# Kernel tuning notes

Hardware: AMD Instinct MI355X
Metric: run time of the kernel (lower is better)

The kernel has to match this reference:

```python
import math
import jax, jax.numpy as jnp
import numpy as np

EPS = 1e-5
DIM_E = 448
DIM_H = 64
TOTAL = DIM_E + DIM_H  # 512
C = 1.0


def _project(x, c, margin=1e-3):
    sqrt_c = jnp.sqrt(c)
    norm = jnp.maximum(jnp.linalg.norm(x, axis=-1, keepdims=True), EPS)
    scale = jnp.minimum(((1.0 - margin) / sqrt_c) / norm, 1.0)
    return x * scale


def _mobius_add(x, y, c):
    x2 = jnp.sum(x * x, axis=-1, keepdims=True)
    y2 = jnp.sum(y * y, axis=-1, keepdims=True)
    xy = jnp.sum(x * y, axis=-1, keepdims=True)
    num = (1.0 + 2.0 * c * xy + c * y2) * x + (1.0 - c * x2) * y
    den = jnp.maximum(1.0 + 2.0 * c * xy + c * c * x2 * y2, EPS)
    return _project(num / den, c)


def _exp0(v, c):
    sqrt_c = jnp.sqrt(c)
    norm = jnp.maximum(jnp.linalg.norm(v, axis=-1, keepdims=True), EPS)
    return _project(jnp.tanh(sqrt_c * norm) * v / (sqrt_c * norm), c)


def _dist(x, y, c):
    # x, y broadcast to [B,S,S,dim_h]; returns [B,S,S]
    sqrt_c = jnp.sqrt(c)
    diff = _mobius_add(-x, y, c)
    norm = jnp.minimum(jnp.linalg.norm(diff, axis=-1), (1.0 - 1e-5) / sqrt_c)
    return (2.0 / sqrt_c) * jnp.arctanh(jnp.minimum(sqrt_c * norm, 1.0 - 1e-5))


def setup_inputs() -> dict:
    key = jax.random.key(0)
    ks = jax.random.split(key, 10)
    B, S = 1, 1024
    s = 1.0 / math.sqrt(TOTAL)
    inp = {
        "x": jax.random.normal(ks[0], (B, S, TOTAL), jnp.float32),
        "wq": jax.random.uniform(ks[1], (TOTAL, TOTAL), jnp.float32, -s, s),
        "bq": jax.random.uniform(ks[2], (TOTAL,), jnp.float32, -s, s),
        "wk": jax.random.uniform(ks[3], (TOTAL, TOTAL), jnp.float32, -s, s),
        "bk": jax.random.uniform(ks[4], (TOTAL,), jnp.float32, -s, s),
        "wv": jax.random.uniform(ks[5], (TOTAL, TOTAL), jnp.float32, -s, s),
        "bv": jax.random.uniform(ks[6], (TOTAL,), jnp.float32, -s, s),
        "wo": jax.random.uniform(ks[7], (TOTAL, TOTAL), jnp.float32, -s, s),
        "bo": jax.random.uniform(ks[8], (TOTAL,), jnp.float32, -s, s),
        "alpha_unconstrained": jnp.float32(0.0),
    }
    return inp


def reference(x, wq, bq, wk, bk, wv, bv, wo, bo, alpha_unconstrained):
    q = x @ wq.T + bq
    k = x @ wk.T + bk
    v = x @ wv.T + bv
    qe, qh = q[..., :DIM_E], q[..., DIM_E:]
    ke, kh = k[..., :DIM_E], k[..., DIM_E:]
    # Euclidean squared distance [B,S,S] via GEMM expansion
    qn = jnp.sum(qe * qe, axis=-1)  # [B,S]
    kn = jnp.sum(ke * ke, axis=-1)  # [B,S]
    d_e = qn[:, :, None] + kn[:, None, :] - 2.0 * jnp.einsum("bsd,btd->bst", qe, ke)
    # Hyperbolic distance on Poincare ball
    qh_h = _exp0(qh, C)
    kh_h = _exp0(kh, C)
    d_h = _dist(qh_h[:, :, None, :], kh_h[:, None, :, :], C)  # [B,S,S]
    alpha = jax.nn.softplus(alpha_unconstrained)
    dist = d_e + alpha * d_h * d_h
    logits = jnp.clip(-dist / math.sqrt(float(TOTAL)), -50.0, 0.0)
    attn = jax.nn.softmax(logits, axis=-1)
    out = jnp.einsum("bst,btd->bsd", attn, v)
    return out @ wo.T + bo
```

## Files before the change

kernel.cpp:

```cpp
#include <hip/hip_runtime.h>

#define S_LEN 1024
#define D_TOT 512
#define D_E   448

typedef short bf16x8 __attribute__((ext_vector_type(8)));
typedef float f32x4  __attribute__((ext_vector_type(4)));
typedef unsigned short u16;

__device__ __forceinline__ float frcp(float x) {
  float r; asm("v_rcp_f32 %0, %1" : "=v"(r) : "v"(x)); return r;
}

__device__ __forceinline__ float wave_sum64(float v) {
#pragma unroll
  for (int o = 32; o > 0; o >>= 1) v += __shfl_xor(v, o);
  return v;
}

__device__ __forceinline__ u16 bf16rne(float f) {
  unsigned u = __builtin_bit_cast(unsigned, f);
  return (u16)((u + 0x7fffu + ((u >> 16) & 1u)) >> 16);
}

__device__ __forceinline__ void bsplit(float f, u16 &h, u16 &l) {
  unsigned u  = __builtin_bit_cast(unsigned, f);
  unsigned ur = u + 0x7fffu + ((u >> 16) & 1u);
  h = (u16)(ur >> 16);
  float fh = __builtin_bit_cast(float, ur & 0xffff0000u);
  float r  = f - fh;
  l = bf16rne(r);
}

__device__ __forceinline__ void bsplit8(float4 a, float4 b, uint4 &h, uint4 &l) {
  u16 h0,h1,h2,h3,h4,h5,h6,h7, l0,l1,l2,l3,l4,l5,l6,l7;
  bsplit(a.x,h0,l0); bsplit(a.y,h1,l1); bsplit(a.z,h2,l2); bsplit(a.w,h3,l3);
  bsplit(b.x,h4,l4); bsplit(b.y,h5,l5); bsplit(b.z,h6,l6); bsplit(b.w,h7,l7);
  h.x = (unsigned)h0 | ((unsigned)h1<<16); h.y = (unsigned)h2 | ((unsigned)h3<<16);
  h.z = (unsigned)h4 | ((unsigned)h5<<16); h.w = (unsigned)h6 | ((unsigned)h7<<16);
  l.x = (unsigned)l0 | ((unsigned)l1<<16); l.y = (unsigned)l2 | ((unsigned)l3<<16);
  l.z = (unsigned)l4 | ((unsigned)l5<<16); l.w = (unsigned)l6 | ((unsigned)l7<<16);
}

__device__ __forceinline__ uint4 rne8(float4 a, float4 b) {
  uint4 h;
  h.x = (unsigned)bf16rne(a.x) | ((unsigned)bf16rne(a.y)<<16);
  h.y = (unsigned)bf16rne(a.z) | ((unsigned)bf16rne(a.w)<<16);
  h.z = (unsigned)bf16rne(b.x) | ((unsigned)bf16rne(b.y)<<16);
  h.w = (unsigned)bf16rne(b.z) | ((unsigned)bf16rne(b.w)<<16);
  return h;
}

#define MFMA2(ACC)                                                                              \
  _Pragma("unroll") for (int i_ = 0; i_ < 2; ++i_)                                              \
  _Pragma("unroll") for (int j_ = 0; j_ < 2; ++j_) {                                            \
    ACC[i_][j_] = __builtin_amdgcn_mfma_f32_16x16x32_bf16(fAh[i_], fBh[j_], ACC[i_][j_],0,0,0); \
    ACC[i_][j_] = __builtin_amdgcn_mfma_f32_16x16x32_bf16(fAh[i_], fBl[j_], ACC[i_][j_],0,0,0); \
  }

__global__ __launch_bounds__(512,4) void qkv_mfma(
    const float* __restrict__ x,
    const float* __restrict__ wq, const float* __restrict__ bq,
    const float* __restrict__ wk, const float* __restrict__ bk,
    const float* __restrict__ wv, const float* __restrict__ bv,
    u16* __restrict__ Qch,
    u16* __restrict__ Kch, u16* __restrict__ Kcl,
    u16* __restrict__ vTh, u16* __restrict__ vTl,
    float* __restrict__ qnpart, float* __restrict__ knpart,
    float* __restrict__ uh2a, float* __restrict__ vh2a)
{
  __shared__ __align__(16) u16 stage[2][15360];
  float* fbuf = (float*)stage;
  const int z = blockIdx.z;
  const float* W; const float* bias;
  if (z == 0)      { W = wq; bias = bq; }
  else if (z == 1) { W = wk; bias = bk; }
  else             { W = wv; bias = bv; }
  const int mBase = blockIdx.y << 6, nBase = blockIdx.x << 6;
  const int t = threadIdx.x, lane = t & 63, wave = t >> 6;
  const int kg = t >> 8, sub = t & 255;
  const int srow = sub >> 2, scol = (sub & 3) << 3;
  const int kgw = wave >> 2, wr = (wave >> 1) & 1, wc = wave & 1;

  const float* Ag = x + (size_t)(mBase + srow) * D_TOT + scol + kg * 256;
  const float* Bg = W + (size_t)(nBase + srow) * D_TOT + scol + kg * 256;

  const int sb = kg * 7680 + srow * 40 + scol;
  const int fa = kgw * 7680 + (wr * 32 + (lane & 15)) * 40 + ((lane >> 4) << 3);
  const int fb = kgw * 7680 + 2560 + (wc * 32 + (lane & 15)) * 40 + ((lane >> 4) << 3);

  float4 a0 = *(const float4*)Ag, a1 = *(const float4*)(Ag + 4);
  float4 b0 = *(const float4*)Bg, b1 = *(const float4*)(Bg + 4);
  {
    uint4 hB,lB; bsplit8(b0,b1,hB,lB);
    *(uint4*)&stage[0][sb       ] = rne8(a0,a1);
    *(uint4*)&stage[0][sb + 2560] = hB;
    *(uint4*)&stage[0][sb + 5120] = lB;
  }
  a0 = *(const float4*)(Ag + 32); a1 = *(const float4*)(Ag + 36);
  b0 = *(const float4*)(Bg + 32); b1 = *(const float4*)(Bg + 36);

  f32x4 zero = {0.f,0.f,0.f,0.f};
  f32x4 acc[2][2] = {{zero,zero},{zero,zero}};
#pragma unroll
  for (int r = 0; r < 8; ++r) {
    __syncthreads();
    const u16* bufr = stage[r & 1];
    bf16x8 fAh[2], fBh[2], fBl[2];
#pragma unroll
    for (int i = 0; i < 2; ++i) {
      fAh[i] = *(const bf16x8*)&bufr[fa        + i*640];
      fBh[i] = *(const bf16x8*)&bufr[fb        + i*640];
      fBl[i] = *(const bf16x8*)&bufr[fb + 2560 + i*640];
    }
    if (r + 1 < 8) {
      u16* bufw = stage[(r + 1) & 1];
      uint4 hB,lB; bsplit8(b0,b1,hB,lB);
      *(uint4*)&bufw[sb       ] = rne8(a0,a1);
      *(uint4*)&bufw[sb + 2560] = hB;
      *(uint4*)&bufw[sb + 5120] = lB;
      if (r + 2 < 8) {
        const int o = (r + 2) * 32;
        a0 = *(const float4*)(Ag + o); a1 = *(const float4*)(Ag + o + 4);
        b0 = *(const float4*)(Bg + o); b1 = *(const float4*)(Bg + o + 4);
      }
    }
    MFMA2(acc);
  }

  __syncthreads();
  {
    const int r0 = wr*32 + ((lane>>4)<<2);
    const int c0 = wc*32 + (lane&15);
#pragma unroll
    for (int i = 0; i < 2; ++i)
#pragma unroll
      for (int j = 0; j < 2; ++j)
#pragma unroll
        for (int g = 0; g < 4; ++g)
          fbuf[kgw*4352 + (r0 + i*16 + g)*68 + c0 + j*16] = acc[i][j][g];
  }
  __syncthreads();
  const int erow = wave << 3;
  float val[8];
  {
    const float b = bias[nBase + lane];
#pragma unroll
    for (int r = 0; r < 8; ++r)
      val[r] = fbuf[(erow+r)*68 + lane] + fbuf[4352 + (erow+r)*68 + lane] + b;
  }

  if (z == 2) {
    u16 hh[8], ll[8];
#pragma unroll
    for (int r = 0; r < 8; ++r) bsplit(val[r], hh[r], ll[r]);
    const size_t off = (size_t)(nBase + lane) * S_LEN + mBase + erow;
    ushort4 p0{hh[0],hh[1],hh[2],hh[3]}, p1{hh[4],hh[5],hh[6],hh[7]};
    ushort4 q0{ll[0],ll[1],ll[2],ll[3]}, q1{ll[4],ll[5],ll[6],ll[7]};
    *(ushort4*)(vTh + off) = p0; *(ushort4*)(vTh + off + 4) = p1;
    *(ushort4*)(vTl + off) = q0; *(ushort4*)(vTl + off + 4) = q1;
  } else if (z == 1) {
    if (blockIdx.x < 7) {
#pragma unroll
      for (int r = 0; r < 8; ++r) {
        const int s = mBase + erow + r;
        u16 h,l; bsplit(val[r],h,l);
        Kch[(size_t)s*D_TOT + nBase + lane] = h;
        Kcl[(size_t)s*D_TOT + nBase + lane] = l;
        float p = wave_sum64(val[r]*val[r]);
        if (lane == 0) knpart[s*8 + blockIdx.x] = p;
      }
    } else {
#pragma unroll
      for (int r = 0; r < 8; ++r) {
        const int s = mBase + erow + r;
        float n2 = wave_sum64(val[r]*val[r]);
        float nn = sqrtf(n2);
        float n  = fmaxf(nn, 1e-5f);
        float e2n = __expf(2.f*n);
        float th  = 1.f - 2.f*frcp(e2n + 1.f);
        float rn  = frcp(n);
        float pn  = th * nn * rn;
        float scale = fminf(0.999f * frcp(fmaxf(pn, 1e-5f)), 1.f);
        float u = th * rn * scale * val[r];
        float un = pn * scale;
        u16 h,l; bsplit(u,h,l);
        Kch[(size_t)s*D_TOT + nBase + lane] = h;
        Kcl[(size_t)s*D_TOT + nBase + lane] = l;
        if (lane == 0) vh2a[s] = un*un;
      }
    }
  } else {
    if (blockIdx.x < 7) {
#pragma unroll
      for (int r = 0; r < 8; ++r) {
        const int s = mBase + erow + r;
        Qch[(size_t)s*D_TOT + nBase + lane] = bf16rne(val[r]);
        float p = wave_sum64(val[r]*val[r]);
        if (lane == 0) qnpart[s*8 + blockIdx.x] = p;
      }
    } else {
#pragma unroll
      for (int r = 0; r < 8; ++r) {
        const int s = mBase + erow + r;
        float n2 = wave_sum64(val[r]*val[r]);
        float nn = sqrtf(n2);
        float n  = fmaxf(nn, 1e-5f);
        float e2n = __expf(2.f*n);
        float th  = 1.f - 2.f*frcp(e2n + 1.f);
        float rn  = frcp(n);
        float pn  = th * nn * rn;
        float scale = fminf(0.999f * frcp(fmaxf(pn, 1e-5f)), 1.f);
        float u = th * rn * scale * val[r];
        float un = pn * scale;
        Qch[(size_t)s*D_TOT + nBase + lane] = bf16rne(u);
        if (lane == 0) uh2a[s] = un*un;
      }
    }
  }
}

__global__ __launch_bounds__(512,4) void score_mfma(
    const u16* __restrict__ Qch,
    const u16* __restrict__ Kch, const u16* __restrict__ Kcl,
    const float* __restrict__ qnpart, const float* __restrict__ knpart,
    const float* __restrict__ uh2a, const float* __restrict__ vh2a,
    const float* __restrict__ alpha_u,
    u16* __restrict__ Eh, float* __restrict__ rowpart)
{
  __shared__ __align__(16) char shm_[69632];
  __shared__ float rowscal[256];
  u16* stg = (u16*)shm_;
  float* fbuf = (float*)shm_;
  const int t = threadIdx.x, lane = t & 63, wave = t >> 6;
  const int mBase = blockIdx.y << 6, nBase = blockIdx.x << 6;
  if (t < 64) {
    float s_ = 0.f;
#pragma unroll
    for (int c = 0; c < 7; ++c) s_ += qnpart[(mBase+t)*8 + c];
    rowscal[t] = s_;
  } else if (t < 128) {
    float s_ = 0.f;
#pragma unroll
    for (int c = 0; c < 7; ++c) s_ += knpart[(nBase+t-64)*8 + c];
    rowscal[t] = s_;
  } else if (t < 192) rowscal[t] = uh2a[mBase + t - 128];
  else if (t < 256)   rowscal[t] = vh2a[nBase + t - 192];

  const int kg = t >> 8, sub = t & 255;
  const int srow = sub >> 2, scol = (sub & 3) << 3;
  const int kgw = wave >> 2, wr = (wave >> 1) & 1, wc = wave & 1;
  const u16* Agh = Qch + (size_t)(mBase+srow)*D_TOT + scol;
  const u16* Bgh = Kch + (size_t)(nBase+srow)*D_TOT + scol;
  const u16* Bgl = Kcl + (size_t)(nBase+srow)*D_TOT + scol;

  const int sb  = kg * 7680 + srow * 40 + scol;
  const int fa  = kgw * 7680 + (wr * 32 + (lane & 15)) * 40 + ((lane >> 4) << 3);
  const int fbh = kgw * 7680 + 2560 + (wc * 32 + (lane & 15)) * 40 + ((lane >> 4) << 3);

  int kb = kg * 224;
  uint4 rAh = *(const uint4*)(Agh + kb);
  uint4 rBh = *(const uint4*)(Bgh + kb), rBl = *(const uint4*)(Bgl + kb);
  *(uint4*)&stg[sb       ] = rAh;
  *(uint4*)&stg[sb + 2560] = rBh;
  *(uint4*)&stg[sb + 5120] = rBl;
  kb = kg * 224 + 32;
  rAh = *(const uint4*)(Agh + kb);
  rBh = *(const uint4*)(Bgh + kb); rBl = *(const uint4*)(Bgl + kb);

  f32x4 zero = {0.f,0.f,0.f,0.f};
  f32x4 accE[2][2] = {{zero,zero},{zero,zero}};
  f32x4 accH[2][2] = {{zero,zero},{zero,zero}};
#pragma unroll
  for (int r = 0; r < 8; ++r) {
    __syncthreads();
    const u16* bufr = stg + (r & 1) * 15360;
    bf16x8 fAh[2], fBh[2], fBl[2];
#pragma unroll
    for (int i = 0; i < 2; ++i) {
      fAh[i] = *(const bf16x8*)&bufr[fa         + i*640];
      fBh[i] = *(const bf16x8*)&bufr[fbh        + i*640];
      fBl[i] = *(const bf16x8*)&bufr[fbh + 2560 + i*640];
    }
    if (r + 1 < 8) {
      u16* bufw = stg + ((r + 1) & 1) * 15360;
      *(uint4*)&bufw[sb       ] = rAh;
      *(uint4*)&bufw[sb + 2560] = rBh;
      *(uint4*)&bufw[sb + 5120] = rBl;
      if (r + 2 < 8) {
        const int o = (r + 2 < 7) ? (kg*224 + (r+2)*32) : (448 + kg*32);
        rAh = *(const uint4*)(Agh + o);
        rBh = *(const uint4*)(Bgh + o); rBl = *(const uint4*)(Bgl + o);
      }
    }
    if (r < 7) { MFMA2(accE) } else { MFMA2(accH) }
  }

  __syncthreads();
  {
    const int r0 = wr*32 + ((lane>>4)<<2);
    const int c0 = wc*32 + (lane&15);
#pragma unroll
    for (int i = 0; i < 2; ++i)
#pragma unroll
      for (int j = 0; j < 2; ++j)
#pragma unroll
        for (int g = 0; g < 4; ++g) {
          fbuf[       kgw*4352 + (r0 + i*16 + g)*68 + c0 + j*16] = accE[i][j][g];
          fbuf[8704 + kgw*4352 + (r0 + i*16 + g)*68 + c0 + j*16] = accH[i][j][g];
        }
  }
  __syncthreads();
  const int erow = wave << 3;
  float eE[8], eH[8];
#pragma unroll
  for (int r = 0; r < 8; ++r) {
    eE[r] = fbuf[(erow+r)*68 + lane] + fbuf[4352 + (erow+r)*68 + lane];
    eH[r] = fbuf[8704 + (erow+r)*68 + lane] + fbuf[8704 + 4352 + (erow+r)*68 + lane];
  }

  const float alpha = __logf(1.f + __expf(alpha_u[0]));
  const float inv_s = 0.04419417382415922f;
  const float knl = rowscal[64 + lane], v2 = rowscal[192 + lane];
#pragma unroll
  for (int r = 0; r < 8; ++r) {
    const int s = mBase + erow + r;
    const float qns = rowscal[erow + r], u2 = rowscal[128 + erow + r];
    float de   = qns + knl - 2.f * eE[r];
    float dH   = eH[r];
    float Ac   = 1.f - 2.f*dH + v2;
    float Bc   = 1.f - u2;
    float num2 = Ac*Ac*u2 + Bc*Bc*v2 - 2.f*Ac*Bc*dH;
    float den  = fmaxf(1.f - 2.f*dH + u2*v2, 1e-5f);
    float frac = sqrtf(fmaxf(num2, 0.f)) * frcp(den);
    float nrm  = fminf(frac, 0.999f);
    float dh_  = __logf((1.f + nrm) * frcp(1.f - nrm));
    float dist = de + alpha * dh_ * dh_;
    float lg   = fminf(fmaxf(-dist * inv_s, -50.f), 0.f);
    float e    = __expf(lg);
    Eh[(size_t)s*S_LEN + nBase + lane] = bf16rne(e);
    float rs = wave_sum64(e);
    if (lane == 0) rowpart[s*16 + blockIdx.x] = rs;
  }
}

__global__ __launch_bounds__(512,4) void av_mfma(
    const u16* __restrict__ Eh,
    const u16* __restrict__ vTh, const u16* __restrict__ vTl,
    const float* __restrict__ rowpart,
    u16* __restrict__ out1h)
{
  __shared__ __align__(16) u16 stg[25600];
  __shared__ float rinvl[32];
  float* fbuf = (float*)stg;
  const int t = threadIdx.x, lane = t & 63, wave = t >> 6;
  const int mBase = blockIdx.y << 5, nBase = blockIdx.x << 6;
  if (t < 32) {
    float s_ = 0.f;
#pragma unroll
    for (int c = 0; c < 16; ++c) s_ += rowpart[(mBase+t)*16 + c];
    rinvl[t] = 1.f / s_;
  }
  const int kg = t >> 7, sub = t & 127;
  const int arow = sub >> 2, acol = (sub & 3) << 3;
  const int brow0 = sub >> 2, bcol0 = (sub & 3) << 3;
  const int brow1 = (sub + 128) >> 2, bcol1 = ((sub + 128) & 3) << 3;
  const int kgw = wave >> 1, wc = wave & 1;

  const u16* Ag  = Eh  + (size_t)(mBase+arow)*S_LEN + acol + kg*256;
  const u16* B0h = vTh + (size_t)(nBase+brow0)*S_LEN + bcol0 + kg*256;
  const u16* B0l = vTl + (size_t)(nBase+brow0)*S_LEN + bcol0 + kg*256;
  const u16* B1h = vTh + (size_t)(nBase+brow1)*S_LEN + bcol1 + kg*256;
  const u16* B1l = vTl + (size_t)(nBase+brow1)*S_LEN + bcol1 + kg*256;

  const int sA  = kg*6400 + arow*40 + acol;
  const int sB0 = kg*6400 + 1280 + brow0*40 + bcol0;
  const int sB1 = kg*6400 + 1280 + brow1*40 + bcol1;
  const int fa  = kgw*6400 + (lane&15)*40 + ((lane>>4)<<3);
  const int fbh = kgw*6400 + 1280 + (wc*32 + (lane&15))*40 + ((lane>>4)<<3);

  uint4 rA = *(const uint4*)Ag;
  uint4 rb0h = *(const uint4*)B0h, rb0l = *(const uint4*)B0l;
  uint4 rb1h = *(const uint4*)B1h, rb1l = *(const uint4*)B1l;

  f32x4 zero = {0.f,0.f,0.f,0.f};
  f32x4 acc[2][2] = {{zero,zero},{zero,zero}};
#pragma unroll
  for (int r = 0; r < 8; ++r) {
    __syncthreads();
    *(uint4*)&stg[sA        ] = rA;
    *(uint4*)&stg[sB0       ] = rb0h; *(uint4*)&stg[sB0 + 2560] = rb0l;
    *(uint4*)&stg[sB1       ] = rb1h; *(uint4*)&stg[sB1 + 2560] = rb1l;
    if (r + 1 < 8) {
      const int o = (r + 1) * 32;
      rA = *(const uint4*)(Ag + o);
      rb0h = *(const uint4*)(B0h + o); rb0l = *(const uint4*)(B0l + o);
      rb1h = *(const uint4*)(B1h + o); rb1l = *(const uint4*)(B1l + o);
    }
    __syncthreads();
    bf16x8 fAh[2], fBh[2], fBl[2];
#pragma unroll
    for (int i = 0; i < 2; ++i) {
      fAh[i] = *(const bf16x8*)&stg[fa         + i*640];
      fBh[i] = *(const bf16x8*)&stg[fbh        + i*640];
      fBl[i] = *(const bf16x8*)&stg[fbh + 2560 + i*640];
    }
    MFMA2(acc);
  }

  __syncthreads();
  {
    const int r0 = (lane>>4)<<2;
    const int c0 = wc*32 + (lane&15);
#pragma unroll
    for (int i = 0; i < 2; ++i)
#pragma unroll
      for (int j = 0; j < 2; ++j)
#pragma unroll
        for (int g = 0; g < 4; ++g)
          fbuf[kgw*2176 + (r0 + i*16 + g)*68 + c0 + j*16] = acc[i][j][g];
  }
  __syncthreads();
  const int erow = wave << 2;
#pragma unroll
  for (int r = 0; r < 4; ++r) {
    const int row = erow + r;
    float e = fbuf[row*68 + lane] + fbuf[2176 + row*68 + lane]
            + fbuf[4352 + row*68 + lane] + fbuf[6528 + row*68 + lane];
    float v_ = e * rinvl[row];
    const int s = mBase + row;
    out1h[(size_t)s*D_TOT + nBase + lane] = bf16rne(v_);
  }
}

__global__ __launch_bounds__(512,4) void final_mfma(
    const u16* __restrict__ out1h,
    const float* __restrict__ wo, const float* __restrict__ bo,
    float* __restrict__ out)
{
  __shared__ __align__(16) u16 stg[25600];
  float* fbuf = (float*)stg;
  const int t = threadIdx.x, lane = t & 63, wave = t >> 6;
  const int mBase = blockIdx.y << 5, nBase = blockIdx.x << 6;
  const int kg = t >> 7, sub = t & 127;
  const int arow = sub >> 2, acol = (sub & 3) << 3;
  const int brow0 = sub >> 2, bcol0 = (sub & 3) << 3;
  const int brow1 = (sub + 128) >> 2, bcol1 = ((sub + 128) & 3) << 3;
  const int kgw = wave >> 1, wc = wave & 1;

  const u16* Ag = out1h + (size_t)(mBase+arow)*D_TOT + acol + kg*128;
  const float* B0 = wo + (size_t)(nBase+brow0)*D_TOT + bcol0 + kg*128;
  const float* B1 = wo + (size_t)(nBase+brow1)*D_TOT + bcol1 + kg*128;

  const int sA  = kg*6400 + arow*40 + acol;
  const int sB0 = kg*6400 + 1280 + brow0*40 + bcol0;
  const int sB1 = kg*6400 + 1280 + brow1*40 + bcol1;
  const int fa  = kgw*6400 + (lane&15)*40 + ((lane>>4)<<3);
  const int fbh = kgw*6400 + 1280 + (wc*32 + (lane&15))*40 + ((lane>>4)<<3);

  uint4 rA = *(const uint4*)Ag;
  float4 b00 = *(const float4*)B0, b01 = *(const float4*)(B0 + 4);
  float4 b10 = *(const float4*)B1, b11 = *(const float4*)(B1 + 4);

  f32x4 zero = {0.f,0.f,0.f,0.f};
  f32x4 acc[2][2] = {{zero,zero},{zero,zero}};
#pragma unroll
  for (int r = 0; r < 4; ++r) {
    __syncthreads();
    uint4 bh0,bl0,bh1,bl1;
    bsplit8(b00,b01,bh0,bl0); bsplit8(b10,b11,bh1,bl1);
    *(uint4*)&stg[sA        ] = rA;
    *(uint4*)&stg[sB0       ] = bh0; *(uint4*)&stg[sB0 + 2560] = bl0;
    *(uint4*)&stg[sB1       ] = bh1; *(uint4*)&stg[sB1 + 2560] = bl1;
    if (r + 1 < 4) {
      const int o = (r + 1) * 32;
      rA = *(const uint4*)(Ag + o);
      b00 = *(const float4*)(B0 + o); b01 = *(const float4*)(B0 + o + 4);
      b10 = *(const float4*)(B1 + o); b11 = *(const float4*)(B1 + o + 4);
    }
    __syncthreads();
    bf16x8 fAh[2], fBh[2], fBl[2];
#pragma unroll
    for (int i = 0; i < 2; ++i) {
      fAh[i] = *(const bf16x8*)&stg[fa         + i*640];
      fBh[i] = *(const bf16x8*)&stg[fbh        + i*640];
      fBl[i] = *(const bf16x8*)&stg[fbh + 2560 + i*640];
    }
    MFMA2(acc);
  }

  __syncthreads();
  {
    const int r0 = (lane>>4)<<2;
    const int c0 = wc*32 + (lane&15);
#pragma unroll
    for (int i = 0; i < 2; ++i)
#pragma unroll
      for (int j = 0; j < 2; ++j)
#pragma unroll
        for (int g = 0; g < 4; ++g)
          fbuf[kgw*2176 + (r0 + i*16 + g)*68 + c0 + j*16] = acc[i][j][g];
  }
  __syncthreads();
  const int erow = wave << 2;
  const float b = bo[nBase + lane];
#pragma unroll
  for (int r = 0; r < 4; ++r) {
    const int row = erow + r;
    float e = fbuf[row*68 + lane] + fbuf[2176 + row*68 + lane]
            + fbuf[4352 + row*68 + lane] + fbuf[6528 + row*68 + lane];
    out[(size_t)(mBase+row)*D_TOT + nBase + lane] = e + b;
  }
}

extern "C" void kernel_launch(void* const* d_in, const int* in_sizes, int n_in,
                              void* d_out, int out_size, void* d_ws, size_t ws_size,
                              hipStream_t stream)
{
  const float* x   = (const float*)d_in[0];
  const float* wq  = (const float*)d_in[1];
  const float* bq  = (const float*)d_in[2];
  const float* wk  = (const float*)d_in[3];
  const float* bk  = (const float*)d_in[4];
  const float* wv  = (const float*)d_in[5];
  const float* bv  = (const float*)d_in[6];
  const float* wo  = (const float*)d_in[7];
  const float* bo  = (const float*)d_in[8];
  const float* alpha_u = (const float*)d_in[9];
  float* out = (float*)d_out;

  u16* U = (u16*)d_ws;
  u16* Qch   = U + 0;
  u16* Kch   = U + 524288;
  u16* Kcl   = U + 1048576;
  u16* vTh   = U + 1572864;
  u16* vTl   = U + 2097152;
  u16* Eh    = U + 2621440;
  u16* out1h = U + 3670016;
  float* F = (float*)(U + 4194304);
  float* qnpart  = F;
  float* knpart  = F + 8192;
  float* uh2a    = F + 16384;
  float* vh2a    = F + 17408;
  float* rowpart = F + 18432;

  qkv_mfma<<<dim3(8,16,3), 512, 0, stream>>>(x, wq,bq, wk,bk, wv,bv,
      Qch, Kch, Kcl, vTh, vTl, qnpart, knpart, uh2a, vh2a);
  score_mfma<<<dim3(16,16), 512, 0, stream>>>(Qch, Kch, Kcl,
      qnpart, knpart, uh2a, vh2a, alpha_u, Eh, rowpart);
  av_mfma<<<dim3(8,32), 512, 0, stream>>>(Eh, vTh, vTl, rowpart, out1h);
  final_mfma<<<dim3(8,32), 512, 0, stream>>>(out1h, wo, bo, out);
}
```

Baseline: 42.07 us.

## Fold output projection into value weights, fusing attention-V and final GEMM

A new kernel precomputes Wo·Wv and Wo·bv. The QKV kernel then produces V already projected by the output weights, and a single av2 kernel applies softmax normalisation and the output bias, so the separate final GEMM launch goes away. The value operand is now stored as bf16 high part only, not hi/lo split, which halves MFMA work and traffic in the attention-V product. That stage also gets double-buffered LDS staging. The cost is an extra small GEMM launch on weights every call and lower precision in the V path.

```diff
diff --git a/kernel.cpp b/kernel.cpp
--- a/kernel.cpp
+++ b/kernel.cpp
@@ -58,14 +58,109 @@
     ACC[i_][j_] = __builtin_amdgcn_mfma_f32_16x16x32_bf16(fAh[i_], fBl[j_], ACC[i_][j_],0,0,0); \
   }
 
+#define MFMA1(ACC)                                                                              \
+  _Pragma("unroll") for (int i_ = 0; i_ < 2; ++i_)                                              \
+  _Pragma("unroll") for (int j_ = 0; j_ < 2; ++j_)                                              \
+    ACC[i_][j_] = __builtin_amdgcn_mfma_f32_16x16x32_bf16(fAh[i_], fBh[j_], ACC[i_][j_],0,0,0);
+
+__global__ __launch_bounds__(512,4) void wprod_mfma(
+    const float* __restrict__ wo, const float* __restrict__ wv,
+    const float* __restrict__ bv,
+    float* __restrict__ W2, float* __restrict__ bvo)
+{
+  __shared__ __align__(16) char shm_[34816];
+  u16* stg = (u16*)shm_;
+  float* fbuf = (float*)shm_;
+  const int t = threadIdx.x, lane = t & 63, wave = t >> 6;
+  const int mBase = blockIdx.y << 6, nBase = blockIdx.x << 6;
+  const int kg = t >> 8, sub = t & 255;
+  const int kgw = wave >> 2, wr = (wave >> 1) & 1, wc = wave & 1;
+
+  const int srow = sub >> 2, scol = (sub & 3) << 3;
+  const float* Ag = wo + (size_t)(mBase + srow) * D_TOT + kg * 256 + scol;
+  const int bk = sub & 31, bng = sub >> 5;
+  const float* Bg = wv + (size_t)(kg * 256 + bk) * D_TOT + nBase + bng * 8;
+
+  const int sA  = kg * 7680 + srow * 40 + scol;
+  const int sBh = kg * 7680 + 2560;
+  const int sBl = kg * 7680 + 5120;
+  const int fa  = kgw * 7680 + (wr * 32 + (lane & 15)) * 40 + ((lane >> 4) << 3);
+  const int fbh = kgw * 7680 + 2560 + (wc * 32 + (lane & 15)) * 40 + ((lane >> 4) << 3);
+
+  f32x4 zero = {0.f,0.f,0.f,0.f};
+  f32x4 acc[2][2] = {{zero,zero},{zero,zero}};
+#pragma unroll
+  for (int r = 0; r < 8; ++r) {
+    float4 a0 = *(const float4*)(Ag + r*32);
+    float4 a1 = *(const float4*)(Ag + r*32 + 4);
+    float4 w0 = *(const float4*)(Bg + (size_t)r*32*D_TOT);
+    float4 w1 = *(const float4*)(Bg + (size_t)r*32*D_TOT + 4);
+    __syncthreads();
+    *(uint4*)&stg[sA] = rne8(a0, a1);
+    float bb[8] = {w0.x,w0.y,w0.z,w0.w,w1.x,w1.y,w1.z,w1.w};
+#pragma unroll
+    for (int j = 0; j < 8; ++j) {
+      u16 h,l; bsplit(bb[j], h, l);
+      stg[sBh + (bng*8 + j)*40 + bk] = h;
+      stg[sBl + (bng*8 + j)*40 + bk] = l;
+    }
+    __syncthreads();
+    bf16x8 fAh[2], fBh[2], fBl[2];
+#pragma unroll
+    for (int i = 0; i < 2; ++i) {
+      fAh[i] = *(const bf16x8*)&stg[fa         + i*640];
+      fBh[i] = *(const bf16x8*)&stg[fbh        + i*640];
+      fBl[i] = *(const bf16x8*)&stg[fbh + 2560 + i*640];
+    }
+    MFMA2(acc);
+  }
+
+  __syncthreads();
+  {
+    const int r0 = wr*32 + ((lane>>4)<<2);
+    const int c0 = wc*32 + (lane&15);
+#pragma unroll
+    for (int i = 0; i < 2; ++i)
+#pragma unroll
+      for (int j = 0; j < 2; ++j)
+#pragma unroll
+        for (int g = 0; g < 4; ++g)
+          fbuf[kgw*4352 + (r0 + i*16 + g)*68 + c0 + j*16] = acc[i][j][g];
+  }
+  __syncthreads();
+  const int erow = wave << 3;
+#pragma unroll
+  for (int r = 0; r < 8; ++r) {
+    float v = fbuf[(erow+r)*68 + lane] + fbuf[4352 + (erow+r)*68 + lane];
+    W2[(size_t)(mBase + erow + r)*D_TOT + nBase + lane] = v;
+  }
+
+  if (blockIdx.x == 0) {
+    __syncthreads();
+    const int m = t >> 3, sl = t & 7;
+    const float* wrow = wo + (size_t)(mBase + m)*D_TOT + sl*64;
+    float s_ = 0.f;
+#pragma unroll
+    for (int k = 0; k < 64; ++k) s_ += wrow[k] * bv[sl*64 + k];
+    fbuf[m*8 + sl] = s_;
+    __syncthreads();
+    if (t < 64) {
+      float s2 = 0.f;
+#pragma unroll
+      for (int c = 0; c < 8; ++c) s2 += fbuf[t*8 + c];
+      bvo[mBase + t] = s2;
+    }
+  }
+}
+
 __global__ __launch_bounds__(512,4) void qkv_mfma(
     const float* __restrict__ x,
     const float* __restrict__ wq, const float* __restrict__ bq,
     const float* __restrict__ wk, const float* __restrict__ bk,
-    const float* __restrict__ wv, const float* __restrict__ bv,
+    const float* __restrict__ w2, const float* __restrict__ bvo,
     u16* __restrict__ Qch,
     u16* __restrict__ Kch, u16* __restrict__ Kcl,
-    u16* __restrict__ vTh, u16* __restrict__ vTl,
+    u16* __restrict__ voTh,
     float* __restrict__ qnpart, float* __restrict__ knpart,
     float* __restrict__ uh2a, float* __restrict__ vh2a)
 {
@@ -75,7 +170,7 @@
   const float* W; const float* bias;
   if (z == 0)      { W = wq; bias = bq; }
   else if (z == 1) { W = wk; bias = bk; }
-  else             { W = wv; bias = bv; }
+  else             { W = w2; bias = bvo; }
   const int mBase = blockIdx.y << 6, nBase = blockIdx.x << 6;
   const int t = threadIdx.x, lane = t & 63, wave = t >> 6;
   const int kg = t >> 8, sub = t & 255;
@@ -151,14 +246,12 @@
   }
 
   if (z == 2) {
-    u16 hh[8], ll[8];
-#pragma unroll
-    for (int r = 0; r < 8; ++r) bsplit(val[r], hh[r], ll[r]);
+    u16 hh[8];
+#pragma unroll
+    for (int r = 0; r < 8; ++r) hh[r] = bf16rne(val[r]);
     const size_t off = (size_t)(nBase + lane) * S_LEN + mBase + erow;
     ushort4 p0{hh[0],hh[1],hh[2],hh[3]}, p1{hh[4],hh[5],hh[6],hh[7]};
-    ushort4 q0{ll[0],ll[1],ll[2],ll[3]}, q1{ll[4],ll[5],ll[6],ll[7]};
-    *(ushort4*)(vTh + off) = p0; *(ushort4*)(vTh + off + 4) = p1;
-    *(ushort4*)(vTl + off) = q0; *(ushort4*)(vTl + off + 4) = q1;
+    *(ushort4*)(voTh + off) = p0; *(ushort4*)(voTh + off + 4) = p1;
   } else if (z == 1) {
     if (blockIdx.x < 7) {
 #pragma unroll
@@ -344,15 +437,14 @@
   }
 }
 
-__global__ __launch_bounds__(512,4) void av_mfma(
-    const u16* __restrict__ Eh,
-    const u16* __restrict__ vTh, const u16* __restrict__ vTl,
-    const float* __restrict__ rowpart,
-    u16* __restrict__ out1h)
+__global__ __launch_bounds__(512,4) void av2_mfma(
+    const u16* __restrict__ Eh, const u16* __restrict__ voTh,
+    const float* __restrict__ rowpart, const float* __restrict__ bo,
+    float* __restrict__ out)
 {
-  __shared__ __align__(16) u16 stg[25600];
+  __shared__ __align__(16) u16 stage[2][15360];
   __shared__ float rinvl[32];
-  float* fbuf = (float*)stg;
+  float* fbuf = (float*)stage;
   const int t = threadIdx.x, lane = t & 63, wave = t >> 6;
   const int mBase = blockIdx.y << 5, nBase = blockIdx.x << 6;
   if (t < 32) {
@@ -363,49 +455,49 @@
   }
   const int kg = t >> 7, sub = t & 127;
   const int arow = sub >> 2, acol = (sub & 3) << 3;
-  const int brow0 = sub >> 2, bcol0 = (sub & 3) << 3;
-  const int brow1 = (sub + 128) >> 2, bcol1 = ((sub + 128) & 3) << 3;
+  const int brow0 = sub >> 2, brow1 = 32 + (sub >> 2), bcol = (sub & 3) << 3;
   const int kgw = wave >> 1, wc = wave & 1;
 
-  const u16* Ag  = Eh  + (size_t)(mBase+arow)*S_LEN + acol + kg*256;
-  const u16* B0h = vTh + (size_t)(nBase+brow0)*S_LEN + bcol0 + kg*256;
-  const u16* B0l = vTl + (size_t)(nBase+brow0)*S_LEN + bcol0 + kg*256;
-  const u16* B1h = vTh + (size_t)(nBase+brow1)*S_LEN + bcol1 + kg*256;
-  const u16* B1l = vTl + (size_t)(nBase+brow1)*S_LEN + bcol1 + kg*256;
-
-  const int sA  = kg*6400 + arow*40 + acol;
-  const int sB0 = kg*6400 + 1280 + brow0*40 + bcol0;
-  const int sB1 = kg*6400 + 1280 + brow1*40 + bcol1;
-  const int fa  = kgw*6400 + (lane&15)*40 + ((lane>>4)<<3);
-  const int fbh = kgw*6400 + 1280 + (wc*32 + (lane&15))*40 + ((lane>>4)<<3);
+  const u16* Ag = Eh   + (size_t)(mBase+arow)*S_LEN + kg*256 + acol;
+  const u16* B0 = voTh + (size_t)(nBase+brow0)*S_LEN + kg*256 + bcol;
+  const u16* B1 = voTh + (size_t)(nBase+brow1)*S_LEN + kg*256 + bcol;
+
+  const int sA  = kg*3840 + arow*40 + acol;
+  const int sB0 = kg*3840 + 1280 + brow0*40 + bcol;
+  const int sB1 = kg*3840 + 1280 + brow1*40 + bcol;
+  const int fa  = kgw*3840 + (lane&15)*40 + ((lane>>4)<<3);
+  const int fb  = kgw*3840 + 1280 + (wc*32 + (lane&15))*40 + ((lane>>4)<<3);
 
   uint4 rA = *(const uint4*)Ag;
-  uint4 rb0h = *(const uint4*)B0h, rb0l = *(const uint4*)B0l;
-  uint4 rb1h = *(const uint4*)B1h, rb1l = *(const uint4*)B1l;
+  uint4 rb0 = *(const uint4*)B0, rb1 = *(const uint4*)B1;
+  *(uint4*)&stage[0][sA ] = rA;
+  *(uint4*)&stage[0][sB0] = rb0; *(uint4*)&stage[0][sB1] = rb1;
+  rA = *(const uint4*)(Ag + 32);
+  rb0 = *(const uint4*)(B0 + 32); rb1 = *(const uint4*)(B1 + 32);
 
   f32x4 zero = {0.f,0.f,0.f,0.f};
   f32x4 acc[2][2] = {{zero,zero},{zero,zero}};
 #pragma unroll
   for (int r = 0; r < 8; ++r) {
     __syncthreads();
-    *(uint4*)&stg[sA        ] = rA;
-    *(uint4*)&stg[sB0       ] = rb0h; *(uint4*)&stg[sB0 + 2560] = rb0l;
-    *(uint4*)&stg[sB1       ] = rb1h; *(uint4*)&stg[sB1 + 2560] = rb1l;
+    const u16* bufr = stage[r & 1];
+    bf16x8 fAh[2], fBh[2];
+#pragma unroll
+    for (int i = 0; i < 2; ++i) {
+      fAh[i] = *(const bf16x8*)&bufr[fa + i*640];
+      fBh[i] = *(const bf16x8*)&bufr[fb + i*640];
+    }
     if (r + 1 < 8) {
-      const int o = (r + 1) * 32;
-      rA = *(const uint4*)(Ag + o);
-      rb0h = *(const uint4*)(B0h + o); rb0l = *(const uint4*)(B0l + o);
-      rb1h = *(const uint4*)(B1h + o); rb1l = *(const uint4*)(B1l + o);
-    }
-    __syncthreads();
-    bf16x8 fAh[2], fBh[2], fBl[2];
-#pragma unroll
-    for (int i = 0; i < 2; ++i) {
-      fAh[i] = *(const bf16x8*)&stg[fa         + i*640];
-      fBh[i] = *(const bf16x8*)&stg[fbh        + i*640];
-      fBl[i] = *(const bf16x8*)&stg[fbh + 2560 + i*640];
-    }
-    MFMA2(acc);
+      u16* bufw = stage[(r + 1) & 1];
+      *(uint4*)&bufw[sA ] = rA;
+      *(uint4*)&bufw[sB0] = rb0; *(uint4*)&bufw[sB1] = rb1;
+      if (r + 2 < 8) {
+        const int o = (r + 2) * 32;
+        rA = *(const uint4*)(Ag + o);
+        rb0 = *(const uint4*)(B0 + o); rb1 = *(const uint4*)(B1 + o);
+      }
+    }
+    MFMA1(acc);
   }
 
   __syncthreads();
@@ -422,94 +514,13 @@
   }
   __syncthreads();
   const int erow = wave << 2;
+  const float b = bo[nBase + lane];
 #pragma unroll
   for (int r = 0; r < 4; ++r) {
     const int row = erow + r;
     float e = fbuf[row*68 + lane] + fbuf[2176 + row*68 + lane]
             + fbuf[4352 + row*68 + lane] + fbuf[6528 + row*68 + lane];
-    float v_ = e * rinvl[row];
-    const int s = mBase + row;
-    out1h[(size_t)s*D_TOT + nBase + lane] = bf16rne(v_);
-  }
-}
-
-__global__ __launch_bounds__(512,4) void final_mfma(
-    const u16* __restrict__ out1h,
-    const float* __restrict__ wo, const float* __restrict__ bo,
-    float* __restrict__ out)
-{
-  __shared__ __align__(16) u16 stg[25600];
-  float* fbuf = (float*)stg;
-  const int t = threadIdx.x, lane = t & 63, wave = t >> 6;
-  const int mBase = blockIdx.y << 5, nBase = blockIdx.x << 6;
-  const int kg = t >> 7, sub = t & 127;
-  const int arow = sub >> 2, acol = (sub & 3) << 3;
-  const int brow0 = sub >> 2, bcol0 = (sub & 3) << 3;
-  const int brow1 = (sub + 128) >> 2, bcol1 = ((sub + 128) & 3) << 3;
-  const int kgw = wave >> 1, wc = wave & 1;
-
-  const u16* Ag = out1h + (size_t)(mBase+arow)*D_TOT + acol + kg*128;
-  const float* B0 = wo + (size_t)(nBase+brow0)*D_TOT + bcol0 + kg*128;
-  const float* B1 = wo + (size_t)(nBase+brow1)*D_TOT + bcol1 + kg*128;
-
-  const int sA  = kg*6400 + arow*40 + acol;
-  const int sB0 = kg*6400 + 1280 + brow0*40 + bcol0;
-  const int sB1 = kg*6400 + 1280 + brow1*40 + bcol1;
-  const int fa  = kgw*6400 + (lane&15)*40 + ((lane>>4)<<3);
-  const int fbh = kgw*6400 + 1280 + (wc*32 + (lane&15))*40 + ((lane>>4)<<3);
-
-  uint4 rA = *(const uint4*)Ag;
-  float4 b00 = *(const float4*)B0, b01 = *(const float4*)(B0 + 4);
-  float4 b10 = *(const float4*)B1, b11 = *(const float4*)(B1 + 4);
-
-  f32x4 zero = {0.f,0.f,0.f,0.f};
-  f32x4 acc[2][2] = {{zero,zero},{zero,zero}};
-#pragma unroll
-  for (int r = 0; r < 4; ++r) {
-    __syncthreads();
-    uint4 bh0,bl0,bh1,bl1;
-    bsplit8(b00,b01,bh0,bl0); bsplit8(b10,b11,bh1,bl1);
-    *(uint4*)&stg[sA        ] = rA;
-    *(uint4*)&stg[sB0       ] = bh0; *(uint4*)&stg[sB0 + 2560] = bl0;
-    *(uint4*)&stg[sB1       ] = bh1; *(uint4*)&stg[sB1 + 2560] = bl1;
-    if (r + 1 < 4) {
-      const int o = (r + 1) * 32;
-      rA = *(const uint4*)(Ag + o);
-      b00 = *(const float4*)(B0 + o); b01 = *(const float4*)(B0 + o + 4);
-      b10 = *(const float4*)(B1 + o); b11 = *(const float4*)(B1 + o + 4);
-    }
-    __syncthreads();
-    bf16x8 fAh[2], fBh[2], fBl[2];
-#pragma unroll
-    for (int i = 0; i < 2; ++i) {
-      fAh[i] = *(const bf16x8*)&stg[fa         + i*640];
-      fBh[i] = *(const bf16x8*)&stg[fbh        + i*640];
-      fBl[i] = *(const bf16x8*)&stg[fbh + 2560 + i*640];
-    }
-    MFMA2(acc);
-  }
-
-  __syncthreads();
-  {
-    const int r0 = (lane>>4)<<2;
-    const int c0 = wc*32 + (lane&15);
-#pragma unroll
-    for (int i = 0; i < 2; ++i)
-#pragma unroll
-      for (int j = 0; j < 2; ++j)
-#pragma unroll
-        for (int g = 0; g < 4; ++g)
-          fbuf[kgw*2176 + (r0 + i*16 + g)*68 + c0 + j*16] = acc[i][j][g];
-  }
-  __syncthreads();
-  const int erow = wave << 2;
-  const float b = bo[nBase + lane];
-#pragma unroll
-  for (int r = 0; r < 4; ++r) {
-    const int row = erow + r;
-    float e = fbuf[row*68 + lane] + fbuf[2176 + row*68 + lane]
-            + fbuf[4352 + row*68 + lane] + fbuf[6528 + row*68 + lane];
-    out[(size_t)(mBase+row)*D_TOT + nBase + lane] = e + b;
+    out[(size_t)(mBase+row)*D_TOT + nBase + lane] = e * rinvl[row] + b;
   }
 }
 
@@ -533,21 +544,21 @@
   u16* Qch   = U + 0;
   u16* Kch   = U + 524288;
   u16* Kcl   = U + 1048576;
-  u16* vTh   = U + 1572864;
-  u16* vTl   = U + 2097152;
-  u16* Eh    = U + 2621440;
-  u16* out1h = U + 3670016;
-  float* F = (float*)(U + 4194304);
-  float* qnpart  = F;
-  float* knpart  = F + 8192;
-  float* uh2a    = F + 16384;
-  float* vh2a    = F + 17408;
-  float* rowpart = F + 18432;
-
-  qkv_mfma<<<dim3(8,16,3), 512, 0, stream>>>(x, wq,bq, wk,bk, wv,bv,
-      Qch, Kch, Kcl, vTh, vTl, qnpart, knpart, uh2a, vh2a);
+  u16* voTh  = U + 1572864;
+  u16* Eh    = U + 2097152;
+  float* F = (float*)(U + 3145728);
+  float* W2      = F;
+  float* bvo     = F + 262144;
+  float* qnpart  = F + 262656;
+  float* knpart  = F + 270848;
+  float* uh2a    = F + 279040;
+  float* vh2a    = F + 280064;
+  float* rowpart = F + 281088;
+
+  wprod_mfma<<<dim3(8,8), 512, 0, stream>>>(wo, wv, bv, W2, bvo);
+  qkv_mfma<<<dim3(8,16,3), 512, 0, stream>>>(x, wq,bq, wk,bk, W2, bvo,
+      Qch, Kch, Kcl, voTh, qnpart, knpart, uh2a, vh2a);
   score_mfma<<<dim3(16,16), 512, 0, stream>>>(Qch, Kch, Kcl,
       qnpart, knpart, uh2a, vh2a, alpha_u, Eh, rowpart);
-  av_mfma<<<dim3(8,32), 512, 0, stream>>>(Eh, vTh, vTl, rowpart, out1h);
-  final_mfma<<<dim3(8,32), 512, 0, stream>>>(out1h, wo, bo, out);
-}
+  av2_mfma<<<dim3(8,32), 512, 0, stream>>>(Eh, voTh, rowpart, bo, out);
+}
```

After: 51.16 us. 21.6% more time.

## Halve score and AV tile sizes to double grid, double-buffer AV staging

Applied to the files above, without the earlier changes.

The score kernel now uses 32x64 output tiles instead of 64x64, launching 512 blocks instead of 256. The AV kernel uses 32x32 tiles over 512 blocks and switches from two barriers per step to a double-buffered LDS pipeline with a single barrier. The goal is better occupancy of the many CUs on a small problem and less synchronisation stall. In exchange, each block reuses less data, so redundant global loads of K/V and Q/E tiles increase.

```diff
diff --git a/kernel.cpp b/kernel.cpp
--- a/kernel.cpp
+++ b/kernel.cpp
@@ -228,106 +228,114 @@
     const float* __restrict__ alpha_u,
     u16* __restrict__ Eh, float* __restrict__ rowpart)
 {
-  __shared__ __align__(16) char shm_[69632];
-  __shared__ float rowscal[256];
+  __shared__ __align__(16) char shm_[51200];
+  __shared__ float rowscal[192];
   u16* stg = (u16*)shm_;
   float* fbuf = (float*)shm_;
   const int t = threadIdx.x, lane = t & 63, wave = t >> 6;
-  const int mBase = blockIdx.y << 6, nBase = blockIdx.x << 6;
-  if (t < 64) {
+  const int mBase = blockIdx.y << 5, nBase = blockIdx.x << 6;
+  if (t < 32) {
     float s_ = 0.f;
 #pragma unroll
     for (int c = 0; c < 7; ++c) s_ += qnpart[(mBase+t)*8 + c];
     rowscal[t] = s_;
-  } else if (t < 128) {
+  } else if (t < 96) {
     float s_ = 0.f;
 #pragma unroll
-    for (int c = 0; c < 7; ++c) s_ += knpart[(nBase+t-64)*8 + c];
+    for (int c = 0; c < 7; ++c) s_ += knpart[(nBase+t-32)*8 + c];
     rowscal[t] = s_;
-  } else if (t < 192) rowscal[t] = uh2a[mBase + t - 128];
-  else if (t < 256)   rowscal[t] = vh2a[nBase + t - 192];
+  } else if (t < 128) rowscal[t] = uh2a[mBase + t - 96];
+  else if (t < 192)   rowscal[t] = vh2a[nBase + t - 128];
 
   const int kg = t >> 8, sub = t & 255;
-  const int srow = sub >> 2, scol = (sub & 3) << 3;
-  const int kgw = wave >> 2, wr = (wave >> 1) & 1, wc = wave & 1;
-  const u16* Agh = Qch + (size_t)(mBase+srow)*D_TOT + scol;
-  const u16* Bgh = Kch + (size_t)(nBase+srow)*D_TOT + scol;
-  const u16* Bgl = Kcl + (size_t)(nBase+srow)*D_TOT + scol;
-
-  const int sb  = kg * 7680 + srow * 40 + scol;
-  const int fa  = kgw * 7680 + (wr * 32 + (lane & 15)) * 40 + ((lane >> 4) << 3);
-  const int fbh = kgw * 7680 + 2560 + (wc * 32 + (lane & 15)) * 40 + ((lane >> 4) << 3);
+  const int wkg = wave >> 2, wc = wave & 3;
+  const int arow = sub >> 3, acol4 = (sub & 7) << 2;
+  const int brow = sub >> 2, bcol8 = (sub & 3) << 3;
+
+  const u16* Agh = Qch + (size_t)(mBase + arow)*D_TOT + acol4;
+  const u16* Bgh = Kch + (size_t)(nBase + brow)*D_TOT + bcol8;
+  const u16* Bgl = Kcl + (size_t)(nBase + brow)*D_TOT + bcol8;
+
+  const int sA  = kg*6400 + arow*40 + acol4;
+  const int sBh = kg*6400 + 1280 + brow*40 + bcol8;
+  const int sBl = kg*6400 + 3840 + brow*40 + bcol8;
+  const int fa  = wkg*6400 + (lane&15)*40 + ((lane>>4)<<3);
+  const int fbh = wkg*6400 + 1280 + (wc*16 + (lane&15))*40 + ((lane>>4)<<3);
+  const int fbl = wkg*6400 + 3840 + (wc*16 + (lane&15))*40 + ((lane>>4)<<3);
 
   int kb = kg * 224;
-  uint4 rAh = *(const uint4*)(Agh + kb);
+  uint2 rA  = *(const uint2*)(Agh + kb);
   uint4 rBh = *(const uint4*)(Bgh + kb), rBl = *(const uint4*)(Bgl + kb);
-  *(uint4*)&stg[sb       ] = rAh;
-  *(uint4*)&stg[sb + 2560] = rBh;
-  *(uint4*)&stg[sb + 5120] = rBl;
+  *(uint2*)&stg[sA ] = rA;
+  *(uint4*)&stg[sBh] = rBh;
+  *(uint4*)&stg[sBl] = rBl;
   kb = kg * 224 + 32;
-  rAh = *(const uint4*)(Agh + kb);
+  rA  = *(const uint2*)(Agh + kb);
   rBh = *(const uint4*)(Bgh + kb); rBl = *(const uint4*)(Bgl + kb);
 
   f32x4 zero = {0.f,0.f,0.f,0.f};
-  f32x4 accE[2][2] = {{zero,zero},{zero,zero}};
-  f32x4 accH[2][2] = {{zero,zero},{zero,zero}};
+  f32x4 accE[2] = {zero, zero};
+  f32x4 accH[2] = {zero, zero};
 #pragma unroll
   for (int r = 0; r < 8; ++r) {
     __syncthreads();
-    const u16* bufr = stg + (r & 1) * 15360;
-    bf16x8 fAh[2], fBh[2], fBl[2];
-#pragma unroll
-    for (int i = 0; i < 2; ++i) {
-      fAh[i] = *(const bf16x8*)&bufr[fa         + i*640];
-      fBh[i] = *(const bf16x8*)&bufr[fbh        + i*640];
-      fBl[i] = *(const bf16x8*)&bufr[fbh + 2560 + i*640];
-    }
+    const u16* bufr = stg + (r & 1) * 12800;
+    bf16x8 fAh[2], fBhv, fBlv;
+    fAh[0] = *(const bf16x8*)&bufr[fa];
+    fAh[1] = *(const bf16x8*)&bufr[fa + 640];
+    fBhv   = *(const bf16x8*)&bufr[fbh];
+    fBlv   = *(const bf16x8*)&bufr[fbl];
     if (r + 1 < 8) {
-      u16* bufw = stg + ((r + 1) & 1) * 15360;
-      *(uint4*)&bufw[sb       ] = rAh;
-      *(uint4*)&bufw[sb + 2560] = rBh;
-      *(uint4*)&bufw[sb + 5120] = rBl;
+      u16* bufw = stg + ((r + 1) & 1) * 12800;
+      *(uint2*)&bufw[sA ] = rA;
+      *(uint4*)&bufw[sBh] = rBh;
+      *(uint4*)&bufw[sBl] = rBl;
       if (r + 2 < 8) {
         const int o = (r + 2 < 7) ? (kg*224 + (r+2)*32) : (448 + kg*32);
-        rAh = *(const uint4*)(Agh + o);
+        rA  = *(const uint2*)(Agh + o);
         rBh = *(const uint4*)(Bgh + o); rBl = *(const uint4*)(Bgl + o);
       }
     }
-    if (r < 7) { MFMA2(accE) } else { MFMA2(accH) }
+    if (r < 7) {
+#pragma unroll
+      for (int i = 0; i < 2; ++i) {
+        accE[i] = __builtin_amdgcn_mfma_f32_16x16x32_bf16(fAh[i], fBhv, accE[i], 0,0,0);
+        accE[i] = __builtin_amdgcn_mfma_f32_16x16x32_bf16(fAh[i], fBlv, accE[i], 0,0,0);
+      }
+    } else {
+#pragma unroll
+      for (int i = 0; i < 2; ++i) {
+        accH[i] = __builtin_amdgcn_mfma_f32_16x16x32_bf16(fAh[i], fBhv, accH[i], 0,0,0);
+        accH[i] = __builtin_amdgcn_mfma_f32_16x16x32_bf16(fAh[i], fBlv, accH[i], 0,0,0);
+      }
+    }
   }
 
   __syncthreads();
   {
-    const int r0 = wr*32 + ((lane>>4)<<2);
-    const int c0 = wc*32 + (lane&15);
+    const int r0 = (lane>>4)<<2;
+    const int c0 = wc*16 + (lane&15);
 #pragma unroll
     for (int i = 0; i < 2; ++i)
 #pragma unroll
-      for (int j = 0; j < 2; ++j)
-#pragma unroll
-        for (int g = 0; g < 4; ++g) {
-          fbuf[       kgw*4352 + (r0 + i*16 + g)*68 + c0 + j*16] = accE[i][j][g];
-          fbuf[8704 + kgw*4352 + (r0 + i*16 + g)*68 + c0 + j*16] = accH[i][j][g];
-        }
-  }
-  __syncthreads();
-  const int erow = wave << 3;
-  float eE[8], eH[8];
-#pragma unroll
-  for (int r = 0; r < 8; ++r) {
-    eE[r] = fbuf[(erow+r)*68 + lane] + fbuf[4352 + (erow+r)*68 + lane];
-    eH[r] = fbuf[8704 + (erow+r)*68 + lane] + fbuf[8704 + 4352 + (erow+r)*68 + lane];
-  }
+      for (int g = 0; g < 4; ++g) {
+        fbuf[       wkg*2176 + (i*16 + r0 + g)*68 + c0] = accE[i][g];
+        fbuf[4352 + wkg*2176 + (i*16 + r0 + g)*68 + c0] = accH[i][g];
+      }
+  }
+  __syncthreads();
 
   const float alpha = __logf(1.f + __expf(alpha_u[0]));
   const float inv_s = 0.04419417382415922f;
-  const float knl = rowscal[64 + lane], v2 = rowscal[192 + lane];
-#pragma unroll
-  for (int r = 0; r < 8; ++r) {
-    const int s = mBase + erow + r;
-    const float qns = rowscal[erow + r], u2 = rowscal[128 + erow + r];
-    float de   = qns + knl - 2.f * eE[r];
-    float dH   = eH[r];
+  const float knl = rowscal[32 + lane], v2 = rowscal[128 + lane];
+#pragma unroll
+  for (int rr = 0; rr < 4; ++rr) {
+    const int row = (wave << 2) + rr;
+    const int s = mBase + row;
+    float eE = fbuf[row*68 + lane] + fbuf[2176 + row*68 + lane];
+    float dH = fbuf[4352 + row*68 + lane] + fbuf[6528 + row*68 + lane];
+    const float qns = rowscal[row], u2 = rowscal[96 + row];
+    float de   = qns + knl - 2.f * eE;
     float Ac   = 1.f - 2.f*dH + v2;
     float Bc   = 1.f - u2;
     float num2 = Ac*Ac*u2 + Bc*Bc*v2 - 2.f*Ac*Bc*dH;
@@ -350,11 +358,12 @@
     const float* __restrict__ rowpart,
     u16* __restrict__ out1h)
 {
-  __shared__ __align__(16) u16 stg[25600];
+  __shared__ __align__(16) char shm_[61440];
   __shared__ float rinvl[32];
-  float* fbuf = (float*)stg;
+  u16* stg = (u16*)shm_;
+  float* fbuf = (float*)shm_;
   const int t = threadIdx.x, lane = t & 63, wave = t >> 6;
-  const int mBase = blockIdx.y << 5, nBase = blockIdx.x << 6;
+  const int mBase = blockIdx.y << 5, nBase = blockIdx.x << 5;
   if (t < 32) {
     float s_ = 0.f;
 #pragma unroll
@@ -362,74 +371,78 @@
     rinvl[t] = 1.f / s_;
   }
   const int kg = t >> 7, sub = t & 127;
-  const int arow = sub >> 2, acol = (sub & 3) << 3;
-  const int brow0 = sub >> 2, bcol0 = (sub & 3) << 3;
-  const int brow1 = (sub + 128) >> 2, bcol1 = ((sub + 128) & 3) << 3;
-  const int kgw = wave >> 1, wc = wave & 1;
-
-  const u16* Ag  = Eh  + (size_t)(mBase+arow)*S_LEN + acol + kg*256;
-  const u16* B0h = vTh + (size_t)(nBase+brow0)*S_LEN + bcol0 + kg*256;
-  const u16* B0l = vTl + (size_t)(nBase+brow0)*S_LEN + bcol0 + kg*256;
-  const u16* B1h = vTh + (size_t)(nBase+brow1)*S_LEN + bcol1 + kg*256;
-  const u16* B1l = vTl + (size_t)(nBase+brow1)*S_LEN + bcol1 + kg*256;
-
-  const int sA  = kg*6400 + arow*40 + acol;
-  const int sB0 = kg*6400 + 1280 + brow0*40 + bcol0;
-  const int sB1 = kg*6400 + 1280 + brow1*40 + bcol1;
-  const int fa  = kgw*6400 + (lane&15)*40 + ((lane>>4)<<3);
-  const int fbh = kgw*6400 + 1280 + (wc*32 + (lane&15))*40 + ((lane>>4)<<3);
-
-  uint4 rA = *(const uint4*)Ag;
-  uint4 rb0h = *(const uint4*)B0h, rb0l = *(const uint4*)B0l;
-  uint4 rb1h = *(const uint4*)B1h, rb1l = *(const uint4*)B1l;
+  const int wc = wave & 1;
+  const int ar = sub >> 2, ac8 = (sub & 3) << 3;
+
+  const u16* Ag = Eh  + (size_t)(mBase + ar)*S_LEN + kg*256 + ac8;
+  const u16* Bh = vTh + (size_t)(nBase + ar)*S_LEN + kg*256 + ac8;
+  const u16* Bl = vTl + (size_t)(nBase + ar)*S_LEN + kg*256 + ac8;
+
+  const int sA  = kg*3840 + ar*40 + ac8;
+  const int sBh = kg*3840 + 1280 + ar*40 + ac8;
+  const int sBl = kg*3840 + 2560 + ar*40 + ac8;
+  const int fa  = kg*3840 + (lane&15)*40 + ((lane>>4)<<3);
+  const int fbh = kg*3840 + 1280 + (wc*16 + (lane&15))*40 + ((lane>>4)<<3);
+  const int fbl = kg*3840 + 2560 + (wc*16 + (lane&15))*40 + ((lane>>4)<<3);
+
+  uint4 rA  = *(const uint4*)Ag;
+  uint4 rBh = *(const uint4*)Bh, rBl = *(const uint4*)Bl;
+  *(uint4*)&stg[sA ] = rA;
+  *(uint4*)&stg[sBh] = rBh;
+  *(uint4*)&stg[sBl] = rBl;
+  rA  = *(const uint4*)(Ag + 32);
+  rBh = *(const uint4*)(Bh + 32); rBl = *(const uint4*)(Bl + 32);
 
   f32x4 zero = {0.f,0.f,0.f,0.f};
-  f32x4 acc[2][2] = {{zero,zero},{zero,zero}};
+  f32x4 acc[2] = {zero, zero};
 #pragma unroll
   for (int r = 0; r < 8; ++r) {
     __syncthreads();
-    *(uint4*)&stg[sA        ] = rA;
-    *(uint4*)&stg[sB0       ] = rb0h; *(uint4*)&stg[sB0 + 2560] = rb0l;
-    *(uint4*)&stg[sB1       ] = rb1h; *(uint4*)&stg[sB1 + 2560] = rb1l;
+    const u16* bufr = stg + (r & 1) * 15360;
+    bf16x8 fAh[2], fBhv, fBlv;
+    fAh[0] = *(const bf16x8*)&bufr[fa];
+    fAh[1] = *(const bf16x8*)&bufr[fa + 640];
+    fBhv   = *(const bf16x8*)&bufr[fbh];
+    fBlv   = *(const bf16x8*)&bufr[fbl];
     if (r + 1 < 8) {
-      const int o = (r + 1) * 32;
-      rA = *(const uint4*)(Ag + o);
-      rb0h = *(const uint4*)(B0h + o); rb0l = *(const uint4*)(B0l + o);
-      rb1h = *(const uint4*)(B1h + o); rb1l = *(const uint4*)(B1l + o);
-    }
-    __syncthreads();
-    bf16x8 fAh[2], fBh[2], fBl[2];
+      u16* bufw = stg + ((r + 1) & 1) * 15360;
+      *(uint4*)&bufw[sA ] = rA;
+      *(uint4*)&bufw[sBh] = rBh;
+      *(uint4*)&bufw[sBl] = rBl;
+      if (r + 2 < 8) {
+        const int o = (r + 2) * 32;
+        rA  = *(const uint4*)(Ag + o);
+        rBh = *(const uint4*)(Bh + o); rBl = *(const uint4*)(Bl + o);
+      }
+    }
 #pragma unroll
     for (int i = 0; i < 2; ++i) {
-      fAh[i] = *(const bf16x8*)&stg[fa         + i*640];
-      fBh[i] = *(const bf16x8*)&stg[fbh        + i*640];
-      fBl[i] = *(const bf16x8*)&stg[fbh + 2560 + i*640];
-    }
-    MFMA2(acc);
+      acc[i] = __builtin_amdgcn_mfma_f32_16x16x32_bf16(fAh[i], fBhv, acc[i], 0,0,0);
+      acc[i] = __builtin_amdgcn_mfma_f32_16x16x32_bf16(fAh[i], fBlv, acc[i], 0,0,0);
+    }
   }
 
   __syncthreads();
   {
     const int r0 = (lane>>4)<<2;
-    const int c0 = wc*32 + (lane&15);
+    const int c0 = wc*16 + (lane&15);
 #pragma unroll
     for (int i = 0; i < 2; ++i)
 #pragma unroll
-      for (int j = 0; j < 2; ++j)
-#pragma unroll
-        for (int g = 0; g < 4; ++g)
-          fbuf[kgw*2176 + (r0 + i*16 + g)*68 + c0 + j*16] = acc[i][j][g];
-  }
-  __syncthreads();
-  const int erow = wave << 2;
-#pragma unroll
-  for (int r = 0; r < 4; ++r) {
-    const int row = erow + r;
-    float e = fbuf[row*68 + lane] + fbuf[2176 + row*68 + lane]
-            + fbuf[4352 + row*68 + lane] + fbuf[6528 + row*68 + lane];
+      for (int g = 0; g < 4; ++g)
+        fbuf[kg*1152 + (i*16 + r0 + g)*36 + c0] = acc[i][g];
+  }
+  __syncthreads();
+  const int col = lane & 31, half = lane >> 5;
+#pragma unroll
+  for (int rr = 0; rr < 2; ++rr) {
+    const int row = (wave << 2) + (half << 1) + rr;
+    float e = 0.f;
+#pragma unroll
+    for (int g = 0; g < 4; ++g) e += fbuf[g*1152 + row*36 + col];
     float v_ = e * rinvl[row];
     const int s = mBase + row;
-    out1h[(size_t)s*D_TOT + nBase + lane] = bf16rne(v_);
+    out1h[(size_t)s*D_TOT + nBase + col] = bf16rne(v_);
   }
 }
 
@@ -546,8 +559,8 @@
 
   qkv_mfma<<<dim3(8,16,3), 512, 0, stream>>>(x, wq,bq, wk,bk, wv,bv,
       Qch, Kch, Kcl, vTh, vTl, qnpart, knpart, uh2a, vh2a);
-  score_mfma<<<dim3(16,16), 512, 0, stream>>>(Qch, Kch, Kcl,
+  score_mfma<<<dim3(16,32), 512, 0, stream>>>(Qch, Kch, Kcl,
       qnpart, knpart, uh2a, vh2a, alpha_u, Eh, rowpart);
-  av_mfma<<<dim3(8,32), 512, 0, stream>>>(Eh, vTh, vTl, rowpart, out1h);
+  av_mfma<<<dim3(16,32), 512, 0, stream>>>(Eh, vTh, vTl, rowpart, out1h);
   final_mfma<<<dim3(8,32), 512, 0, stream>>>(out1h, wo, bo, out);
 }
```

Result: slower. 43.91 us (+4.4%).
